# Performance work log

Measured on AMD Instinct MI355X. Metric: run time of the kernel, lower is better.

## Reference

```python
import jax, jax.numpy as jnp
import numpy as np
import math

B, S, E, H = 2, 2048, 1024, 16
D = E // H          # d_k = 64 = n_qubits_per_head
F = 1024            # ffn_dim; MUST equal E for the original mixing to broadcast
LN_EPS = 1e-5


def _layernorm(x, g, b):
    m = jnp.mean(x, axis=-1, keepdims=True)
    v = jnp.var(x, axis=-1, keepdims=True)
    return (x - m) / jnp.sqrt(v + LN_EPS) * g + b


def _circuit_expvals(x):
    # Closed form of the variational circuit: RY(x_i) on wire i, RZ(theta_i),
    # CNOT chain (i -> i+1), measure PauliZ on each wire.
    # RZ is diagonal (no effect on Z probs); CNOT chain makes bit_i the XOR of
    # bits 0..i, so <Z_i> = prod_{j<=i} cos(x_j).
    return jnp.cumprod(jnp.cos(x), axis=-1)


def setup_inputs() -> dict:
    key = jax.random.key(0)
    ks = jax.random.split(key, 18)
    sc = 0.02
    inp = {
        "x": jax.random.normal(ks[0], (B, S, E), jnp.float32),
        "mask": jnp.ones((B, S), jnp.int32),
        "wq": jax.random.normal(ks[1], (E, E), jnp.float32) * sc,
        "wk": jax.random.normal(ks[2], (E, E), jnp.float32) * sc,
        "wv": jax.random.normal(ks[3], (E, E), jnp.float32) * sc,
        "wo": jax.random.normal(ks[4], (E, E), jnp.float32) * sc,
        "attn_param": jax.random.normal(ks[5], (D,), jnp.float32),   # RZ angles (no effect on expvals)
        "attn_qw": jnp.float32(0.5),
        "w1": jax.random.normal(ks[6], (E, F), jnp.float32) * sc,
        "b1": jnp.zeros((F,), jnp.float32),
        "w2": jax.random.normal(ks[7], (F, E), jnp.float32) * sc,
        "b2": jnp.zeros((E,), jnp.float32),
        "ffn_param": jax.random.normal(ks[8], (E,), jnp.float32),    # RZ angles (no effect on expvals)
        "ffn_qw": jnp.float32(0.5),
        "ln1_g": jnp.ones((E,), jnp.float32),
        "ln1_b": jnp.zeros((E,), jnp.float32),
        "ln2_g": jnp.ones((E,), jnp.float32),
        "ln2_b": jnp.zeros((E,), jnp.float32),
    }
    return inp


def reference(x, mask, wq, wk, wv, wo, attn_param, attn_qw,
              w1, b1, w2, b2, ffn_param, ffn_qw,
              ln1_g, ln1_b, ln2_g, ln2_b):
    b, s, _ = x.shape
    # ---- quantum attention sublayer (dropout inactive / eval mode) ----
    q = (x @ wq).reshape(b, s, H, D).transpose(0, 2, 1, 3)  # [b,h,s,d]
    k = (x @ wk).reshape(b, s, H, D).transpose(0, 2, 1, 3)
    v = (x @ wv).reshape(b, s, H, D).transpose(0, 2, 1, 3)
    scores = jnp.einsum("bhqd,bhkd->bhqk", q, k) / math.sqrt(D)
    scores = jnp.where(mask[:, None, None, :] == 0, -jnp.inf, scores)
    attn = jax.nn.softmax(scores, axis=-1)
    classical = jnp.einsum("bhqk,bhkd->bhqd", attn, v)
    quantum = _circuit_expvals(q)                             # [b,h,s,d]
    wgt = jax.nn.sigmoid(attn_qw)
    out = wgt * quantum + (1.0 - wgt) * classical
    attn_out = out.transpose(0, 2, 1, 3).reshape(b, s, E) @ wo
    x1 = _layernorm(x + attn_out, ln1_g, ln1_b)
    # ---- quantum feed-forward sublayer ----
    classical2 = jax.nn.relu(x1 @ w1 + b1)                    # [b,s,F]
    quantum2 = _circuit_expvals(x1)                           # [b,s,E] (E==F)
    wgt2 = jax.nn.sigmoid(ffn_qw)
    h = wgt2 * quantum2 + (1.0 - wgt2) * classical2
    ffn_out = h @ w2 + b2
    return _layernorm(x1 + ffn_out, ln2_g, ln2_b)
```

## Files before the change

### kernel.cpp

```cpp
#include <hip/hip_runtime.h>
#include <hip/hip_bf16.h>
#include <cmath>
#include <cstdint>


typedef __bf16 bf16_t;
typedef __bf16 bf16x8 __attribute__((ext_vector_type(8)));
typedef float f32x4 __attribute__((ext_vector_type(4)));
typedef unsigned short u16x4 __attribute__((ext_vector_type(4)));

#define DEV_INLINE __device__ __forceinline__
#define MB 1048576

DEV_INLINE void gload16(const void* g, void* lds) {
  __builtin_amdgcn_global_load_lds(
      (const __attribute__((address_space(1))) unsigned int*)g,
      (__attribute__((address_space(3))) unsigned int*)lds, 16, 0, 0);
}

DEV_INLINE unsigned short bf16_bits(float f) {
  bf16_t b = (bf16_t)f;
  return __builtin_bit_cast(unsigned short, b);
}

__global__ __launch_bounds__(256) void convx_kernel(const float* __restrict__ src,
                                                    bf16_t* __restrict__ dst) {
  const size_t i0 = ((size_t)blockIdx.x * 256 + threadIdx.x) * 8;
  bf16x8 v;
#pragma unroll
  for (int j = 0; j < 8; ++j) v[j] = (bf16_t)src[i0 + j];
  *(bf16x8*)(dst + i0) = v;
}

__global__ __launch_bounds__(256) void tconv3_kernel(const float* __restrict__ w0,
                                                     const float* __restrict__ w1,
                                                     const float* __restrict__ w2,
                                                     bf16_t* __restrict__ dst) {
  __shared__ bf16_t t[32][33];
  const int mi = blockIdx.x >> 5;
  const float* src = (mi == 0) ? w0 : (mi == 1) ? w1 : w2;
  const int bx = (blockIdx.x & 31) * 32, by = blockIdx.y * 32;
  const int tx = threadIdx.x & 31, ty = threadIdx.x >> 5;
#pragma unroll
  for (int i = 0; i < 4; ++i)
    t[ty + i * 8][tx] = (bf16_t)src[(size_t)(by + ty + i * 8) * 1024 + bx + tx];
  __syncthreads();
#pragma unroll
  for (int i = 0; i < 4; ++i)
    dst[(size_t)(mi * 1024 + bx + ty + i * 8) * 1024 + by + tx] = t[tx][ty + i * 8];
}

enum { EPI_QK = 0, EPI_VT = 1, EPI_WO = 2, EPI_W1 = 3, EPI_W2 = 4 };

template <int EPI, int IM>
__global__ __launch_bounds__(256) void gemm_bt_kernel(
    const bf16_t* __restrict__ A, const bf16_t* __restrict__ Bt,
    void* __restrict__ o0, void* __restrict__ o1,
    const float* __restrict__ auxf, const bf16_t* __restrict__ auxb,
    const float* __restrict__ bias, const float* __restrict__ scal) {
  constexpr int K = 1024, BM = IM * 32, BK = 64;
  __shared__ __align__(16) bf16_t As[BM * BK];
  __shared__ __align__(16) bf16_t Bs[128 * BK];

  const int tid = threadIdx.x;
  const int w = tid >> 6, lane = tid & 63;
  const int quad = lane >> 4, tc = lane & 15;
  const int m0 = blockIdx.y * BM, n0 = blockIdx.x * 128;
  const int wm = (w >> 1) * (IM * 16), wn = (w & 1) * 64;
  const int srow = lane >> 3, scol = (lane & 7) * 8;

  f32x4 acc[IM][4] = {};

  const bf16_t* Ab = A + (size_t)m0 * K;
  const bf16_t* Bb = Bt + (size_t)n0 * K;

  for (int k0 = 0; k0 < K; k0 += BK) {
    __syncthreads();
#pragma unroll
    for (int it = 0; it < IM; ++it) {
      const int rbase = w * (IM * 8) + it * 8;
      gload16(Ab + (size_t)(rbase + srow) * K + k0 + scol, &As[rbase * BK]);
    }
#pragma unroll
    for (int it = 0; it < 4; ++it) {
      const int rbase = w * 32 + it * 8;
      gload16(Bb + (size_t)(rbase + srow) * K + k0 + scol, &Bs[rbase * BK]);
    }
    __syncthreads();
#pragma unroll
    for (int ks = 0; ks < 2; ++ks) {
      bf16x8 af[IM], bfv[4];
#pragma unroll
      for (int i = 0; i < IM; ++i)
        af[i] = *(const bf16x8*)&As[(wm + i * 16 + tc) * BK + ks * 32 + quad * 8];
#pragma unroll
      for (int j = 0; j < 4; ++j)
        bfv[j] = *(const bf16x8*)&Bs[(wn + j * 16 + tc) * BK + ks * 32 + quad * 8];
#pragma unroll
      for (int i = 0; i < IM; ++i)
#pragma unroll
        for (int j = 0; j < 4; ++j)
          acc[i][j] = __builtin_amdgcn_mfma_f32_16x16x32_bf16(af[i], bfv[j],
                                                              acc[i][j], 0, 0, 0);
    }
  }

  float wsig = 0.f;
  if (EPI == EPI_W1) wsig = 1.f / (1.f + __expf(-scal[0]));

#pragma unroll
  for (int i = 0; i < IM; ++i) {
#pragma unroll
    for (int j = 0; j < 4; ++j) {
      const int row0 = m0 + wm + i * 16 + quad * 4;
      const int col = n0 + wn + j * 16 + tc;
      if (EPI == EPI_QK) {
        const int part = col >> 10, e = col & 1023, hh = e >> 6, d = e & 63;
        bf16_t* dst = part ? (bf16_t*)o1 : (bf16_t*)o0;
#pragma unroll
        for (int r = 0; r < 4; ++r) {
          const int row = row0 + r;
          const int b = row >> 11, s = row & 2047;
          dst[((size_t)(b * 16 + hh) * 2048 + s) * 64 + d] = (bf16_t)acc[i][j][r];
        }
      } else if (EPI == EPI_VT) {
        const int b = col >> 11, s = col & 2047;
#pragma unroll
        for (int r = 0; r < 4; ++r) {
          ((bf16_t*)o0)[((size_t)(b * 1024 + row0 + r)) * 2048 + s] =
              (bf16_t)acc[i][j][r];
        }
      } else if (EPI == EPI_WO) {
#pragma unroll
        for (int r = 0; r < 4; ++r) {
          const int row = row0 + r;
          ((float*)o0)[(size_t)row * 1024 + col] =
              acc[i][j][r] + auxf[(size_t)row * 1024 + col];
        }
      } else if (EPI == EPI_W1) {
#pragma unroll
        for (int r = 0; r < 4; ++r) {
          const int row = row0 + r;
          float c = fmaxf(acc[i][j][r] + bias[col], 0.f);
          const float qv = (float)auxb[(size_t)row * 1024 + col];
          ((bf16_t*)o0)[(size_t)row * 1024 + col] =
              (bf16_t)(wsig * qv + (1.f - wsig) * c);
        }
      } else {
#pragma unroll
        for (int r = 0; r < 4; ++r) {
          const int row = row0 + r;
          ((float*)o0)[(size_t)row * 1024 + col] =
              acc[i][j][r] + bias[col] + (float)auxb[(size_t)row * 1024 + col];
        }
      }
    }
  }
}

__global__ __launch_bounds__(256) void attn_kernel(
    const bf16_t* __restrict__ q, const bf16_t* __restrict__ k,
    const bf16_t* __restrict__ vT, const float* __restrict__ aqw,
    bf16_t* __restrict__ out) {
  constexpr int S = 2048, LDK = 72;
  __shared__ __align__(16) bf16_t Ks[64 * LDK];
  __shared__ __align__(16) bf16_t Vs[64 * LDK];
  __shared__ __align__(16) bf16_t Ps[4 * 16 * LDK];
  __shared__ bf16_t Ql[64 * LDK];
  __shared__ float segp[64][4];

  const int tid = threadIdx.x, w = tid >> 6, lane = tid & 63;
  const int quad = lane >> 4, tc = lane & 15;
  const int bh = blockIdx.y, q0 = blockIdx.x * 64;
  const bf16_t* qg = q + ((size_t)bh * S + q0) * 64;
  const bf16_t* kg = k + (size_t)bh * S * 64;
  const bf16_t* vg = vT + (size_t)bh * 64 * S;

  {
    const int rr = tid >> 2, ss = tid & 3;
    const bf16_t* qr = qg + rr * 64 + ss * 16;
    float c[16], p = 1.f;
#pragma unroll
    for (int j2 = 0; j2 < 16; ++j2) {
      c[j2] = __cosf((float)qr[j2]);
      p *= c[j2];
    }
    segp[rr][ss] = p;
    __syncthreads();
    float pre = 1.f;
    for (int u = 0; u < ss; ++u) pre *= segp[rr][u];
#pragma unroll
    for (int j2 = 0; j2 < 16; ++j2) {
      pre *= c[j2];
      Ql[rr * LDK + ss * 16 + j2] = (bf16_t)pre;
    }
  }

  bf16x8 aq[2];
  {
    const int qrow = w * 16 + tc;
#pragma unroll
    for (int ks = 0; ks < 2; ++ks) {
      bf16x8 t = *(const bf16x8*)(qg + qrow * 64 + ks * 32 + quad * 8);
#pragma unroll
      for (int e = 0; e < 8; ++e) t[e] = (bf16_t)((float)t[e] * 0.125f);
      aq[ks] = t;
    }
  }

  float lacc = 0.f;
  f32x4 o[4] = {};
  bf16_t* Pw = &Ps[w * 16 * LDK];

  const int strow = tid >> 2, stcol = (tid & 3) * 16;

  for (int kt = 0; kt < S; kt += 64) {
    __syncthreads();
    {
      bf16x8 k0v = *(const bf16x8*)(kg + (size_t)(kt + strow) * 64 + stcol);
      bf16x8 k1v = *(const bf16x8*)(kg + (size_t)(kt + strow) * 64 + stcol + 8);
      bf16x8 v0v = *(const bf16x8*)(vg + (size_t)strow * S + kt + stcol);
      bf16x8 v1v = *(const bf16x8*)(vg + (size_t)strow * S + kt + stcol + 8);
      *(bf16x8*)&Ks[strow * LDK + stcol] = k0v;
      *(bf16x8*)&Ks[strow * LDK + stcol + 8] = k1v;
      *(bf16x8*)&Vs[strow * LDK + stcol] = v0v;
      *(bf16x8*)&Vs[strow * LDK + stcol + 8] = v1v;
    }
    __syncthreads();

    f32x4 sf[4] = {};
#pragma unroll
    for (int ks = 0; ks < 2; ++ks) {
#pragma unroll
      for (int nt = 0; nt < 4; ++nt) {
        bf16x8 ak = *(const bf16x8*)&Ks[(nt * 16 + tc) * LDK + ks * 32 + quad * 8];
        sf[nt] = __builtin_amdgcn_mfma_f32_16x16x32_bf16(ak, aq[ks], sf[nt], 0, 0, 0);
      }
    }

#pragma unroll
    for (int nt = 0; nt < 4; ++nt) {
      u16x4 pk;
      float ps = 0.f;
#pragma unroll
      for (int r = 0; r < 4; ++r) {
        const float p = __expf(sf[nt][r]);
        ps += p;
        pk[r] = bf16_bits(p);
      }
      lacc += ps;
      *(u16x4*)&Pw[tc * LDK + nt * 16 + quad * 4] = pk;
    }
    asm volatile("s_waitcnt lgkmcnt(0)" ::: "memory");

#pragma unroll
    for (int ks = 0; ks < 2; ++ks) {
      bf16x8 ap = *(const bf16x8*)&Pw[tc * LDK + ks * 32 + quad * 8];
#pragma unroll
      for (int j = 0; j < 4; ++j) {
        bf16x8 bv = *(const bf16x8*)&Vs[(j * 16 + tc) * LDK + ks * 32 + quad * 8];
        o[j] = __builtin_amdgcn_mfma_f32_16x16x32_bf16(ap, bv, o[j], 0, 0, 0);
      }
    }
  }

  lacc += __shfl_xor(lacc, 16, 64);
  lacc += __shfl_xor(lacc, 32, 64);

  const float wsig = 1.f / (1.f + __expf(-aqw[0]));
  const int b = bh >> 4, h = bh & 15;
#pragma unroll
  for (int r = 0; r < 4; ++r) {
    const int lr = quad * 4 + r;
    const float linv = 1.f / __shfl(lacc, lr, 64);
    const int sg = q0 + w * 16 + lr;
#pragma unroll
    for (int j = 0; j < 4; ++j) {
      const int d = j * 16 + tc;
      const float cl = o[j][r] * linv;
      const float qv = (float)Ql[(w * 16 + lr) * LDK + d];
      out[((size_t)(b * 2048 + sg)) * 1024 + h * 64 + d] =
          (bf16_t)(wsig * qv + (1.f - wsig) * cl);
    }
  }
}

__global__ __launch_bounds__(256) void ln1scan_kernel(
    const float* __restrict__ res, const float* __restrict__ g,
    const float* __restrict__ bta, bf16_t* __restrict__ x1,
    bf16_t* __restrict__ q2) {
  const int row = blockIdx.x;
  const int tid = threadIdx.x, w = tid >> 6, lane = tid & 63;
  f32x4 v = *(const f32x4*)&res[(size_t)row * 1024 + tid * 4];
  float s = v[0] + v[1] + v[2] + v[3];
  float sq = v[0] * v[0] + v[1] * v[1] + v[2] * v[2] + v[3] * v[3];
#pragma unroll
  for (int off = 32; off >= 1; off >>= 1) {
    s += __shfl_xor(s, off, 64);
    sq += __shfl_xor(sq, off, 64);
  }
  __shared__ float rs[4], rq[4], wtot[4];
  if (lane == 0) {
    rs[w] = s;
    rq[w] = sq;
  }
  __syncthreads();
  s = rs[0] + rs[1] + rs[2] + rs[3];
  sq = rq[0] + rq[1] + rq[2] + rq[3];
  const float mean = s * (1.f / 1024.f);
  const float var = fmaxf(sq * (1.f / 1024.f) - mean * mean, 0.f);
  const float rstd = rsqrtf(var + 1e-5f);

  const f32x4 gv = *(const f32x4*)&g[tid * 4];
  const f32x4 bv = *(const f32x4*)&bta[tid * 4];
  float c[4], p = 1.f;
  u16x4 xb;
#pragma unroll
  for (int i = 0; i < 4; ++i) {
    const float y = (v[i] - mean) * rstd * gv[i] + bv[i];
    const bf16_t yb = (bf16_t)y;
    xb[i] = __builtin_bit_cast(unsigned short, yb);
    c[i] = __cosf((float)yb);
    p *= c[i];
  }
  *(u16x4*)&x1[(size_t)row * 1024 + tid * 4] = xb;

  float ip = p;
#pragma unroll
  for (int off = 1; off < 64; off <<= 1) {
    const float t = __shfl_up(ip, off, 64);
    if (lane >= off) ip *= t;
  }
  if (lane == 63) wtot[w] = ip;
  __syncthreads();
  float carry = 1.f;
  for (int u = 0; u < w; ++u) carry *= wtot[u];
  float run = __shfl_up(ip, 1, 64);
  if (lane == 0) run = 1.f;
  run *= carry;
  u16x4 qv;
#pragma unroll
  for (int i = 0; i < 4; ++i) {
    run *= c[i];
    qv[i] = bf16_bits(run);
  }
  *(u16x4*)&q2[(size_t)row * 1024 + tid * 4] = qv;
}

__global__ __launch_bounds__(256) void ln2_kernel(
    const float* __restrict__ res, const float* __restrict__ g,
    const float* __restrict__ bta, float* __restrict__ out) {
  const int row = blockIdx.x;
  const int tid = threadIdx.x, w = tid >> 6, lane = tid & 63;
  f32x4 v = *(const f32x4*)&res[(size_t)row * 1024 + tid * 4];
  float s = v[0] + v[1] + v[2] + v[3];
  float sq = v[0] * v[0] + v[1] * v[1] + v[2] * v[2] + v[3] * v[3];
#pragma unroll
  for (int off = 32; off >= 1; off >>= 1) {
    s += __shfl_xor(s, off, 64);
    sq += __shfl_xor(sq, off, 64);
  }
  __shared__ float rs[4], rq[4];
  if (lane == 0) {
    rs[w] = s;
    rq[w] = sq;
  }
  __syncthreads();
  s = rs[0] + rs[1] + rs[2] + rs[3];
  sq = rq[0] + rq[1] + rq[2] + rq[3];
  const float mean = s * (1.f / 1024.f);
  const float var = fmaxf(sq * (1.f / 1024.f) - mean * mean, 0.f);
  const float rstd = rsqrtf(var + 1e-5f);
  const f32x4 gv = *(const f32x4*)&g[tid * 4];
  const f32x4 bv = *(const f32x4*)&bta[tid * 4];
  f32x4 y;
#pragma unroll
  for (int i = 0; i < 4; ++i) y[i] = (v[i] - mean) * rstd * gv[i] + bv[i];
  *(f32x4*)&out[(size_t)row * 1024 + tid * 4] = y;
}

extern "C" void kernel_launch(void* const* d_in, const int* in_sizes, int n_in,
                              void* d_out, int out_size, void* d_ws,
                              size_t ws_size, hipStream_t stream) {
  (void)in_sizes;
  (void)n_in;
  (void)out_size;
  (void)ws_size;
  const float* x = (const float*)d_in[0];
  const float* wq = (const float*)d_in[2];
  const float* wk = (const float*)d_in[3];
  const float* wv = (const float*)d_in[4];
  const float* wo = (const float*)d_in[5];
  const float* attn_qw = (const float*)d_in[7];
  const float* w1 = (const float*)d_in[8];
  const float* b1 = (const float*)d_in[9];
  const float* w2 = (const float*)d_in[10];
  const float* b2 = (const float*)d_in[11];
  const float* ffn_qw = (const float*)d_in[13];
  const float* ln1_g = (const float*)d_in[14];
  const float* ln1_b = (const float*)d_in[15];
  const float* ln2_g = (const float*)d_in[16];
  const float* ln2_b = (const float*)d_in[17];

  char* ws = (char*)d_ws;
  char* wsout = (char*)d_out;
  bf16_t* wT3 = (bf16_t*)(ws + 0);
  bf16_t* wqkvT = (bf16_t*)(ws + 6 * MB);
  bf16_t* xc = (bf16_t*)(ws + 12 * MB);
  bf16_t* qb = (bf16_t*)(ws + 20 * MB);
  bf16_t* aout = (bf16_t*)(ws + 6 * MB);
  float* res = (float*)(ws + 14 * MB);
  bf16_t* x1 = (bf16_t*)(ws + 6 * MB);
  float* res2 = (float*)(ws + 14 * MB);
  bf16_t* kb = (bf16_t*)(wsout + 0);
  bf16_t* vTb = (bf16_t*)(wsout + 8 * MB);
  bf16_t* q2 = (bf16_t*)(wsout + 0);
  bf16_t* hbuf = (bf16_t*)(wsout + 8 * MB);

  const dim3 tb(256);

  convx_kernel<<<2048, tb, 0, stream>>>(x, xc);
  tconv3_kernel<<<dim3(96, 32), tb, 0, stream>>>(wq, wk, wv, wqkvT);
  tconv3_kernel<<<dim3(96, 32), tb, 0, stream>>>(wo, w1, w2, wT3);

  gemm_bt_kernel<EPI_QK, 4><<<dim3(16, 32), tb, 0, stream>>>(
      xc, wqkvT, qb, kb, nullptr, nullptr, nullptr, nullptr);
  gemm_bt_kernel<EPI_VT, 2><<<dim3(32, 16), tb, 0, stream>>>(
      wqkvT + 2 * 1024 * 1024, xc, vTb, nullptr, nullptr, nullptr, nullptr, nullptr);

  attn_kernel<<<dim3(32, 32), tb, 0, stream>>>(qb, kb, vTb, attn_qw, aout);

  gemm_bt_kernel<EPI_WO, 2><<<dim3(8, 64), tb, 0, stream>>>(
      aout, wT3, res, nullptr, x, nullptr, nullptr, nullptr);

  ln1scan_kernel<<<4096, tb, 0, stream>>>(res, ln1_g, ln1_b, x1, q2);

  gemm_bt_kernel<EPI_W1, 2><<<dim3(8, 64), tb, 0, stream>>>(
      x1, wT3 + 1024 * 1024, hbuf, nullptr, nullptr, q2, b1, ffn_qw);

  gemm_bt_kernel<EPI_W2, 2><<<dim3(8, 64), tb, 0, stream>>>(
      hbuf, wT3 + 2 * 1024 * 1024, res2, nullptr, nullptr, x1, b2, nullptr);

  ln2_kernel<<<4096, tb, 0, stream>>>(res2, ln2_g, ln2_b, (float*)d_out);
}
```

Before: 309.0 us.

## Merge prep and QKV/VT launches, widen attention blocks to 128 query rows

The x conversion and both weight transpose kernels become a single prep launch, and the QK and VT projection GEMMs are merged into one launch with 128x128 tiles that picks its role from the block index. The attention kernel now processes 128 query rows per block (32 per wave), so each K/V tile loaded into LDS is reused by two query sub-tiles. This cuts launch count and K/V reload traffic, at the cost of more registers and LDS per block and half as many attention blocks, which lowers occupancy and parallelism.

```diff
diff --git a/kernel.cpp b/kernel.cpp
--- a/kernel.cpp
+++ b/kernel.cpp
@@ -23,23 +23,36 @@
   return __builtin_bit_cast(unsigned short, b);
 }
 
-__global__ __launch_bounds__(256) void convx_kernel(const float* __restrict__ src,
-                                                    bf16_t* __restrict__ dst) {
-  const size_t i0 = ((size_t)blockIdx.x * 256 + threadIdx.x) * 8;
-  bf16x8 v;
-#pragma unroll
-  for (int j = 0; j < 8; ++j) v[j] = (bf16_t)src[i0 + j];
-  *(bf16x8*)(dst + i0) = v;
-}
-
-__global__ __launch_bounds__(256) void tconv3_kernel(const float* __restrict__ w0,
-                                                     const float* __restrict__ w1,
-                                                     const float* __restrict__ w2,
-                                                     bf16_t* __restrict__ dst) {
+__global__ __launch_bounds__(256) void prep_kernel(
+    const float* __restrict__ x, const float* __restrict__ wq,
+    const float* __restrict__ wk, const float* __restrict__ wv,
+    const float* __restrict__ wo, const float* __restrict__ w1,
+    const float* __restrict__ w2, bf16_t* __restrict__ xc,
+    bf16_t* __restrict__ wqkvT, bf16_t* __restrict__ wT3) {
   __shared__ bf16_t t[32][33];
-  const int mi = blockIdx.x >> 5;
-  const float* src = (mi == 0) ? w0 : (mi == 1) ? w1 : w2;
-  const int bx = (blockIdx.x & 31) * 32, by = blockIdx.y * 32;
+  const int bid = blockIdx.x;
+  if (bid < 2048) {
+    const size_t i0 = ((size_t)bid * 256 + threadIdx.x) * 8;
+    bf16x8 v;
+#pragma unroll
+    for (int j = 0; j < 8; ++j) v[j] = (bf16_t)x[i0 + j];
+    *(bf16x8*)(xc + i0) = v;
+    return;
+  }
+  const int grp = (bid - 2048) / 3072;
+  const int tcb = (bid - 2048) - grp * 3072;
+  const int mi = tcb >> 10;
+  const float* src;
+  bf16_t* dst;
+  if (grp == 0) {
+    src = (mi == 0) ? wq : (mi == 1) ? wk : wv;
+    dst = wqkvT;
+  } else {
+    src = (mi == 0) ? wo : (mi == 1) ? w1 : w2;
+    dst = wT3;
+  }
+  const int rem = tcb & 1023;
+  const int bx = (rem & 31) * 32, by = (rem >> 5) * 32;
   const int tx = threadIdx.x & 31, ty = threadIdx.x >> 5;
 #pragma unroll
   for (int i = 0; i < 4; ++i)
@@ -50,54 +63,58 @@
     dst[(size_t)(mi * 1024 + bx + ty + i * 8) * 1024 + by + tx] = t[tx][ty + i * 8];
 }
 
-enum { EPI_QK = 0, EPI_VT = 1, EPI_WO = 2, EPI_W1 = 3, EPI_W2 = 4 };
-
-template <int EPI, int IM>
-__global__ __launch_bounds__(256) void gemm_bt_kernel(
-    const bf16_t* __restrict__ A, const bf16_t* __restrict__ Bt,
-    void* __restrict__ o0, void* __restrict__ o1,
-    const float* __restrict__ auxf, const bf16_t* __restrict__ auxb,
-    const float* __restrict__ bias, const float* __restrict__ scal) {
-  constexpr int K = 1024, BM = IM * 32, BK = 64;
-  __shared__ __align__(16) bf16_t As[BM * BK];
+__global__ __launch_bounds__(256) void qkvvt_kernel(
+    const bf16_t* __restrict__ xc, const bf16_t* __restrict__ wqkvT,
+    bf16_t* __restrict__ qb, bf16_t* __restrict__ kb,
+    bf16_t* __restrict__ vTb) {
+  constexpr int K = 1024, BK = 64;
+  __shared__ __align__(16) bf16_t As[128 * BK];
   __shared__ __align__(16) bf16_t Bs[128 * BK];
 
   const int tid = threadIdx.x;
   const int w = tid >> 6, lane = tid & 63;
   const int quad = lane >> 4, tc = lane & 15;
-  const int m0 = blockIdx.y * BM, n0 = blockIdx.x * 128;
-  const int wm = (w >> 1) * (IM * 16), wn = (w & 1) * 64;
+  const int bid = blockIdx.x;
+  const int isqk = (bid < 512);
+  int m0, n0;
+  const bf16_t *Ab, *Bb;
+  if (isqk) {
+    n0 = (bid & 15) * 128;
+    m0 = (bid >> 4) * 128;
+    Ab = xc + (size_t)m0 * K;
+    Bb = wqkvT + (size_t)n0 * K;
+  } else {
+    const int t = bid - 512;
+    n0 = (t & 31) * 128;
+    m0 = (t >> 5) * 128;
+    Ab = wqkvT + (size_t)(2 * 1024 * 1024) + (size_t)m0 * K;
+    Bb = xc + (size_t)n0 * K;
+  }
+  const int wm = (w >> 1) * 64, wn = (w & 1) * 64;
   const int srow = lane >> 3, scol = (lane & 7) * 8;
 
-  f32x4 acc[IM][4] = {};
-
-  const bf16_t* Ab = A + (size_t)m0 * K;
-  const bf16_t* Bb = Bt + (size_t)n0 * K;
+  f32x4 acc[4][4] = {};
 
   for (int k0 = 0; k0 < K; k0 += BK) {
     __syncthreads();
-#pragma unroll
-    for (int it = 0; it < IM; ++it) {
-      const int rbase = w * (IM * 8) + it * 8;
-      gload16(Ab + (size_t)(rbase + srow) * K + k0 + scol, &As[rbase * BK]);
-    }
 #pragma unroll
     for (int it = 0; it < 4; ++it) {
       const int rbase = w * 32 + it * 8;
+      gload16(Ab + (size_t)(rbase + srow) * K + k0 + scol, &As[rbase * BK]);
       gload16(Bb + (size_t)(rbase + srow) * K + k0 + scol, &Bs[rbase * BK]);
     }
     __syncthreads();
 #pragma unroll
     for (int ks = 0; ks < 2; ++ks) {
-      bf16x8 af[IM], bfv[4];
-#pragma unroll
-      for (int i = 0; i < IM; ++i)
+      bf16x8 af[4], bfv[4];
+#pragma unroll
+      for (int i = 0; i < 4; ++i)
         af[i] = *(const bf16x8*)&As[(wm + i * 16 + tc) * BK + ks * 32 + quad * 8];
 #pragma unroll
       for (int j = 0; j < 4; ++j)
         bfv[j] = *(const bf16x8*)&Bs[(wn + j * 16 + tc) * BK + ks * 32 + quad * 8];
 #pragma unroll
-      for (int i = 0; i < IM; ++i)
+      for (int i = 0; i < 4; ++i)
 #pragma unroll
         for (int j = 0; j < 4; ++j)
           acc[i][j] = __builtin_amdgcn_mfma_f32_16x16x32_bf16(af[i], bfv[j],
@@ -105,32 +122,97 @@
     }
   }
 
-  float wsig = 0.f;
-  if (EPI == EPI_W1) wsig = 1.f / (1.f + __expf(-scal[0]));
-
-#pragma unroll
-  for (int i = 0; i < IM; ++i) {
+#pragma unroll
+  for (int i = 0; i < 4; ++i) {
 #pragma unroll
     for (int j = 0; j < 4; ++j) {
       const int row0 = m0 + wm + i * 16 + quad * 4;
       const int col = n0 + wn + j * 16 + tc;
-      if (EPI == EPI_QK) {
+      if (isqk) {
         const int part = col >> 10, e = col & 1023, hh = e >> 6, d = e & 63;
-        bf16_t* dst = part ? (bf16_t*)o1 : (bf16_t*)o0;
+        bf16_t* dst = part ? kb : qb;
 #pragma unroll
         for (int r = 0; r < 4; ++r) {
           const int row = row0 + r;
           const int b = row >> 11, s = row & 2047;
           dst[((size_t)(b * 16 + hh) * 2048 + s) * 64 + d] = (bf16_t)acc[i][j][r];
         }
-      } else if (EPI == EPI_VT) {
+      } else {
         const int b = col >> 11, s = col & 2047;
 #pragma unroll
         for (int r = 0; r < 4; ++r) {
-          ((bf16_t*)o0)[((size_t)(b * 1024 + row0 + r)) * 2048 + s] =
-              (bf16_t)acc[i][j][r];
+          vTb[((size_t)(b * 1024 + row0 + r)) * 2048 + s] = (bf16_t)acc[i][j][r];
         }
-      } else if (EPI == EPI_WO) {
+      }
+    }
+  }
+}
+
+enum { EPI_WO = 2, EPI_W1 = 3, EPI_W2 = 4 };
+
+template <int EPI>
+__global__ __launch_bounds__(256) void gemm_bt_kernel(
+    const bf16_t* __restrict__ A, const bf16_t* __restrict__ Bt,
+    void* __restrict__ o0, const float* __restrict__ auxf,
+    const bf16_t* __restrict__ auxb, const float* __restrict__ bias,
+    const float* __restrict__ scal) {
+  constexpr int K = 1024, IM = 2, BM = 64, BK = 64;
+  __shared__ __align__(16) bf16_t As[BM * BK];
+  __shared__ __align__(16) bf16_t Bs[128 * BK];
+
+  const int tid = threadIdx.x;
+  const int w = tid >> 6, lane = tid & 63;
+  const int quad = lane >> 4, tc = lane & 15;
+  const int m0 = blockIdx.y * BM, n0 = blockIdx.x * 128;
+  const int wm = (w >> 1) * 32, wn = (w & 1) * 64;
+  const int srow = lane >> 3, scol = (lane & 7) * 8;
+
+  f32x4 acc[IM][4] = {};
+
+  const bf16_t* Ab = A + (size_t)m0 * K;
+  const bf16_t* Bb = Bt + (size_t)n0 * K;
+
+  for (int k0 = 0; k0 < K; k0 += BK) {
+    __syncthreads();
+#pragma unroll
+    for (int it = 0; it < IM; ++it) {
+      const int rbase = w * (IM * 8) + it * 8;
+      gload16(Ab + (size_t)(rbase + srow) * K + k0 + scol, &As[rbase * BK]);
+    }
+#pragma unroll
+    for (int it = 0; it < 4; ++it) {
+      const int rbase = w * 32 + it * 8;
+      gload16(Bb + (size_t)(rbase + srow) * K + k0 + scol, &Bs[rbase * BK]);
+    }
+    __syncthreads();
+#pragma unroll
+    for (int ks = 0; ks < 2; ++ks) {
+      bf16x8 af[IM], bfv[4];
+#pragma unroll
+      for (int i = 0; i < IM; ++i)
+        af[i] = *(const bf16x8*)&As[(wm + i * 16 + tc) * BK + ks * 32 + quad * 8];
+#pragma unroll
+      for (int j = 0; j < 4; ++j)
+        bfv[j] = *(const bf16x8*)&Bs[(wn + j * 16 + tc) * BK + ks * 32 + quad * 8];
+#pragma unroll
+      for (int i = 0; i < IM; ++i)
+#pragma unroll
+        for (int j = 0; j < 4; ++j)
+          acc[i][j] = __builtin_amdgcn_mfma_f32_16x16x32_bf16(af[i], bfv[j],
+                                                              acc[i][j], 0, 0, 0);
+    }
+  }
+
+  float wsig = 0.f;
+  if (EPI == EPI_W1) wsig = 1.f / (1.f + __expf(-scal[0]));
+
+#pragma unroll
+  for (int i = 0; i < IM; ++i) {
+#pragma unroll
+    for (int j = 0; j < 4; ++j) {
+      const int row0 = m0 + wm + i * 16 + quad * 4;
+      const int col = n0 + wn + j * 16 + tc;
+      if (EPI == EPI_WO) {
 #pragma unroll
         for (int r = 0; r < 4; ++r) {
           const int row = row0 + r;
@@ -165,52 +247,62 @@
   constexpr int S = 2048, LDK = 72;
   __shared__ __align__(16) bf16_t Ks[64 * LDK];
   __shared__ __align__(16) bf16_t Vs[64 * LDK];
-  __shared__ __align__(16) bf16_t Ps[4 * 16 * LDK];
-  __shared__ bf16_t Ql[64 * LDK];
-  __shared__ float segp[64][4];
+  __shared__ __align__(16) bf16_t Ps[4][32 * LDK];
+  __shared__ bf16_t Ql[128 * LDK];
+  __shared__ float segp[128][4];
 
   const int tid = threadIdx.x, w = tid >> 6, lane = tid & 63;
   const int quad = lane >> 4, tc = lane & 15;
-  const int bh = blockIdx.y, q0 = blockIdx.x * 64;
+  const int bh = blockIdx.y, q0 = blockIdx.x * 128;
   const bf16_t* qg = q + ((size_t)bh * S + q0) * 64;
   const bf16_t* kg = k + (size_t)bh * S * 64;
   const bf16_t* vg = vT + (size_t)bh * 64 * S;
 
   {
-    const int rr = tid >> 2, ss = tid & 3;
-    const bf16_t* qr = qg + rr * 64 + ss * 16;
-    float c[16], p = 1.f;
-#pragma unroll
-    for (int j2 = 0; j2 < 16; ++j2) {
-      c[j2] = __cosf((float)qr[j2]);
-      p *= c[j2];
-    }
-    segp[rr][ss] = p;
-    __syncthreads();
-    float pre = 1.f;
-    for (int u = 0; u < ss; ++u) pre *= segp[rr][u];
-#pragma unroll
-    for (int j2 = 0; j2 < 16; ++j2) {
-      pre *= c[j2];
-      Ql[rr * LDK + ss * 16 + j2] = (bf16_t)pre;
-    }
-  }
-
-  bf16x8 aq[2];
-  {
-    const int qrow = w * 16 + tc;
+    float c[2][16];
+    const int ss = tid & 3;
+#pragma unroll
+    for (int pass = 0; pass < 2; ++pass) {
+      const int rr = pass * 64 + (tid >> 2);
+      const bf16_t* qr = qg + rr * 64 + ss * 16;
+      float p = 1.f;
+#pragma unroll
+      for (int j2 = 0; j2 < 16; ++j2) {
+        c[pass][j2] = __cosf((float)qr[j2]);
+        p *= c[pass][j2];
+      }
+      segp[rr][ss] = p;
+    }
+    __syncthreads();
+#pragma unroll
+    for (int pass = 0; pass < 2; ++pass) {
+      const int rr = pass * 64 + (tid >> 2);
+      float pre = 1.f;
+      for (int u = 0; u < ss; ++u) pre *= segp[rr][u];
+#pragma unroll
+      for (int j2 = 0; j2 < 16; ++j2) {
+        pre *= c[pass][j2];
+        Ql[rr * LDK + ss * 16 + j2] = (bf16_t)pre;
+      }
+    }
+  }
+
+  bf16x8 aq[2][2];
+#pragma unroll
+  for (int qs = 0; qs < 2; ++qs) {
+    const int qrow = w * 32 + qs * 16 + tc;
 #pragma unroll
     for (int ks = 0; ks < 2; ++ks) {
       bf16x8 t = *(const bf16x8*)(qg + qrow * 64 + ks * 32 + quad * 8);
 #pragma unroll
       for (int e = 0; e < 8; ++e) t[e] = (bf16_t)((float)t[e] * 0.125f);
-      aq[ks] = t;
-    }
-  }
-
-  float lacc = 0.f;
-  f32x4 o[4] = {};
-  bf16_t* Pw = &Ps[w * 16 * LDK];
+      aq[qs][ks] = t;
+    }
+  }
+
+  float lacc[2] = {0.f, 0.f};
+  f32x4 o[2][4] = {};
+  bf16_t* Pw = Ps[w];
 
   const int strow = tid >> 2, stcol = (tid & 3) * 16;
 
@@ -228,59 +320,72 @@
     }
     __syncthreads();
 
-    f32x4 sf[4] = {};
+    f32x4 sf[2][4] = {};
 #pragma unroll
     for (int ks = 0; ks < 2; ++ks) {
 #pragma unroll
       for (int nt = 0; nt < 4; ++nt) {
         bf16x8 ak = *(const bf16x8*)&Ks[(nt * 16 + tc) * LDK + ks * 32 + quad * 8];
-        sf[nt] = __builtin_amdgcn_mfma_f32_16x16x32_bf16(ak, aq[ks], sf[nt], 0, 0, 0);
-      }
-    }
-
-#pragma unroll
-    for (int nt = 0; nt < 4; ++nt) {
-      u16x4 pk;
-      float ps = 0.f;
-#pragma unroll
-      for (int r = 0; r < 4; ++r) {
-        const float p = __expf(sf[nt][r]);
-        ps += p;
-        pk[r] = bf16_bits(p);
-      }
-      lacc += ps;
-      *(u16x4*)&Pw[tc * LDK + nt * 16 + quad * 4] = pk;
+        sf[0][nt] = __builtin_amdgcn_mfma_f32_16x16x32_bf16(ak, aq[0][ks], sf[0][nt], 0, 0, 0);
+        sf[1][nt] = __builtin_amdgcn_mfma_f32_16x16x32_bf16(ak, aq[1][ks], sf[1][nt], 0, 0, 0);
+      }
+    }
+
+#pragma unroll
+    for (int qs = 0; qs < 2; ++qs) {
+#pragma unroll
+      for (int nt = 0; nt < 4; ++nt) {
+        u16x4 pk;
+        float ps = 0.f;
+#pragma unroll
+        for (int r = 0; r < 4; ++r) {
+          const float p = __expf(sf[qs][nt][r]);
+          ps += p;
+          pk[r] = bf16_bits(p);
+        }
+        lacc[qs] += ps;
+        *(u16x4*)&Pw[(qs * 16 + tc) * LDK + nt * 16 + quad * 4] = pk;
+      }
     }
     asm volatile("s_waitcnt lgkmcnt(0)" ::: "memory");
 
 #pragma unroll
     for (int ks = 0; ks < 2; ++ks) {
-      bf16x8 ap = *(const bf16x8*)&Pw[tc * LDK + ks * 32 + quad * 8];
+      bf16x8 ap0 = *(const bf16x8*)&Pw[tc * LDK + ks * 32 + quad * 8];
+      bf16x8 ap1 = *(const bf16x8*)&Pw[(16 + tc) * LDK + ks * 32 + quad * 8];
 #pragma unroll
       for (int j = 0; j < 4; ++j) {
         bf16x8 bv = *(const bf16x8*)&Vs[(j * 16 + tc) * LDK + ks * 32 + quad * 8];
-        o[j] = __builtin_amdgcn_mfma_f32_16x16x32_bf16(ap, bv, o[j], 0, 0, 0);
-      }
-    }
-  }
-
-  lacc += __shfl_xor(lacc, 16, 64);
-  lacc += __shfl_xor(lacc, 32, 64);
+        o[0][j] = __builtin_amdgcn_mfma_f32_16x16x32_bf16(ap0, bv, o[0][j], 0, 0, 0);
+        o[1][j] = __builtin_amdgcn_mfma_f32_16x16x32_bf16(ap1, bv, o[1][j], 0, 0, 0);
+      }
+    }
+  }
+
+#pragma unroll
+  for (int qs = 0; qs < 2; ++qs) {
+    lacc[qs] += __shfl_xor(lacc[qs], 16, 64);
+    lacc[qs] += __shfl_xor(lacc[qs], 32, 64);
+  }
 
   const float wsig = 1.f / (1.f + __expf(-aqw[0]));
   const int b = bh >> 4, h = bh & 15;
 #pragma unroll
-  for (int r = 0; r < 4; ++r) {
-    const int lr = quad * 4 + r;
-    const float linv = 1.f / __shfl(lacc, lr, 64);
-    const int sg = q0 + w * 16 + lr;
-#pragma unroll
-    for (int j = 0; j < 4; ++j) {
-      const int d = j * 16 + tc;
-      const float cl = o[j][r] * linv;
-      const float qv = (float)Ql[(w * 16 + lr) * LDK + d];
-      out[((size_t)(b * 2048 + sg)) * 1024 + h * 64 + d] =
-          (bf16_t)(wsig * qv + (1.f - wsig) * cl);
+  for (int qs = 0; qs < 2; ++qs) {
+#pragma unroll
+    for (int r = 0; r < 4; ++r) {
+      const int lr = quad * 4 + r;
+      const float linv = 1.f / __shfl(lacc[qs], lr, 64);
+      const int lrow = w * 32 + qs * 16 + lr;
+      const int sg = q0 + lrow;
+#pragma unroll
+      for (int j = 0; j < 4; ++j) {
+        const int d = j * 16 + tc;
+        const float cl = o[qs][j][r] * linv;
+        const float qv = (float)Ql[lrow * LDK + d];
+        out[((size_t)(b * 2048 + sg)) * 1024 + h * 64 + d] =
+            (bf16_t)(wsig * qv + (1.f - wsig) * cl);
+      }
     }
   }
 }
@@ -419,27 +524,22 @@
 
   const dim3 tb(256);
 
-  convx_kernel<<<2048, tb, 0, stream>>>(x, xc);
-  tconv3_kernel<<<dim3(96, 32), tb, 0, stream>>>(wq, wk, wv, wqkvT);
-  tconv3_kernel<<<dim3(96, 32), tb, 0, stream>>>(wo, w1, w2, wT3);
-
-  gemm_bt_kernel<EPI_QK, 4><<<dim3(16, 32), tb, 0, stream>>>(
-      xc, wqkvT, qb, kb, nullptr, nullptr, nullptr, nullptr);
-  gemm_bt_kernel<EPI_VT, 2><<<dim3(32, 16), tb, 0, stream>>>(
-      wqkvT + 2 * 1024 * 1024, xc, vTb, nullptr, nullptr, nullptr, nullptr, nullptr);
-
-  attn_kernel<<<dim3(32, 32), tb, 0, stream>>>(qb, kb, vTb, attn_qw, aout);
-
-  gemm_bt_kernel<EPI_WO, 2><<<dim3(8, 64), tb, 0, stream>>>(
-      aout, wT3, res, nullptr, x, nullptr, nullptr, nullptr);
+  prep_kernel<<<8192, tb, 0, stream>>>(x, wq, wk, wv, wo, w1, w2, xc, wqkvT, wT3);
+
+  qkvvt_kernel<<<768, tb, 0, stream>>>(xc, wqkvT, qb, kb, vTb);
+
+  attn_kernel<<<dim3(16, 32), tb, 0, stream>>>(qb, kb, vTb, attn_qw, aout);
+
+  gemm_bt_kernel<EPI_WO><<<dim3(8, 64), tb, 0, stream>>>(
+      aout, wT3, res, x, nullptr, nullptr, nullptr);
 
   ln1scan_kernel<<<4096, tb, 0, stream>>>(res, ln1_g, ln1_b, x1, q2);
 
-  gemm_bt_kernel<EPI_W1, 2><<<dim3(8, 64), tb, 0, stream>>>(
-      x1, wT3 + 1024 * 1024, hbuf, nullptr, nullptr, q2, b1, ffn_qw);
-
-  gemm_bt_kernel<EPI_W2, 2><<<dim3(8, 64), tb, 0, stream>>>(
-      hbuf, wT3 + 2 * 1024 * 1024, res2, nullptr, nullptr, x1, b2, nullptr);
+  gemm_bt_kernel<EPI_W1><<<dim3(8, 64), tb, 0, stream>>>(
+      x1, wT3 + 1024 * 1024, hbuf, nullptr, q2, b1, ffn_qw);
+
+  gemm_bt_kernel<EPI_W2><<<dim3(8, 64), tb, 0, stream>>>(
+      hbuf, wT3 + 2 * 1024 * 1024, res2, nullptr, x1, b2, nullptr);
 
   ln2_kernel<<<4096, tb, 0, stream>>>(res2, ln2_g, ln2_b, (float*)d_out);
 }
```

Measured after the change: 303.7 us. No clear change (-1.7%).
